# Kernel optimization log

Measured on AMD Instinct MI355X. Metric: run time of the kernel, lower is better.

## Reference

```python
import jax, jax.numpy as jnp
import numpy as np
import math

B, T, C = 2, 2048, 1024
NH = 16
HD = C // NH

def setup_inputs() -> dict:
    key = jax.random.key(0)
    ks = jax.random.split(key, 3)
    scale = 0.02
    return {
        "x": jax.random.normal(ks[0], (B, T, C), dtype=jnp.float32),
        "Wqkv": jax.random.normal(ks[1], (C, 3 * C), dtype=jnp.float32) * scale,
        "bqkv": jnp.zeros((3 * C,), dtype=jnp.float32),
        "Wproj": jax.random.normal(ks[2], (C, C), dtype=jnp.float32) * scale,
        "bproj": jnp.zeros((C,), dtype=jnp.float32),
    }

def reference(x, Wqkv, bqkv, Wproj, bproj):
    b, t, c = x.shape
    qkv = x @ Wqkv + bqkv                      # (B,T,3C)
    qkv = qkv.reshape(b, t, 3, NH, HD)
    q = jnp.transpose(qkv[:, :, 0], (0, 2, 1, 3))  # (B,H,T,D)
    k = jnp.transpose(qkv[:, :, 1], (0, 2, 1, 3))
    v = jnp.transpose(qkv[:, :, 2], (0, 2, 1, 3))
    att = jnp.einsum('bhqd,bhkd->bhqk', q, k) / math.sqrt(HD)
    causal = jnp.tril(jnp.ones((t, t), dtype=bool))
    att = jnp.where(causal[None, None], att, jnp.float32(-jnp.inf))
    att = jax.nn.softmax(att, axis=-1)
    y = jnp.einsum('bhqk,bhkd->bhqd', att, v)  # (B,H,T,D)
    y = jnp.transpose(y, (0, 2, 1, 3)).reshape(b, t, c)
    return y @ Wproj + bproj
```

## Files before the change

kernel.cpp:

```cpp
#include <hip/hip_runtime.h>


typedef __attribute__((ext_vector_type(8))) short short8;
typedef __attribute__((ext_vector_type(4))) float f32x4;
struct ushort4_t { unsigned short x, y, z, w; };

#define MFMA16(a, b, c) __builtin_amdgcn_mfma_f32_16x16x32_bf16((a), (b), (c), 0, 0, 0)

__device__ __forceinline__ unsigned short f2bf(float f) {
  unsigned u = __builtin_bit_cast(unsigned, f);
  u += 0x7fffu + ((u >> 16) & 1u);
  return (unsigned short)(u >> 16);
}

__device__ __forceinline__ unsigned short f2bf_fast(float f) {
  return (unsigned short)((__builtin_bit_cast(unsigned, f) + 0x8000u) >> 16);
}

__device__ __forceinline__ void gl2lds16(const void* g, void* l) {
  __builtin_amdgcn_global_load_lds(
      (__attribute__((address_space(1))) void*)g,
      (__attribute__((address_space(3))) void*)l,
      16, 0, 0);
}

__global__ __launch_bounds__(256) void conv_bf16(const float* __restrict__ src,
                                                 unsigned short* __restrict__ dst,
                                                 int n) {
  int i = (blockIdx.x * 256 + threadIdx.x) * 4;
  if (i >= n) return;
  float4 f = *(const float4*)(src + i);
  unsigned long long r = (unsigned long long)f2bf(f.x)
      | ((unsigned long long)f2bf(f.y) << 16)
      | ((unsigned long long)f2bf(f.z) << 32)
      | ((unsigned long long)f2bf(f.w) << 48);
  *(unsigned long long*)(dst + i) = r;
}

__global__ __launch_bounds__(256) void transpose_conv(const float* __restrict__ W,
                                                      unsigned short* __restrict__ WT,
                                                      int K, int N) {
  __shared__ float tile[64][65];
  const int n0 = blockIdx.x * 64, k0 = blockIdx.y * 64;
  const int tid = threadIdx.x;
  const int c = tid & 63, rbase = tid >> 6;
#pragma unroll
  for (int i = 0; i < 16; ++i) {
    int r = i * 4 + rbase;
    tile[r][c] = W[(size_t)(k0 + r) * N + n0 + c];
  }
  __syncthreads();
#pragma unroll
  for (int i = 0; i < 16; ++i) {
    int r = i * 4 + rbase;
    WT[(size_t)(n0 + r) * K + k0 + c] = f2bf(tile[c][r]);
  }
}

template <int EPI, int MT>
__global__ __launch_bounds__(256)
void gemm_bt(const unsigned short* __restrict__ A,
             const unsigned short* __restrict__ BT,
             const float* __restrict__ bias,
             float* __restrict__ outF,
             unsigned short* __restrict__ q_out,
             unsigned short* __restrict__ k_out,
             unsigned short* __restrict__ vT_out,
             int Ndim, int Kdim) {
  constexpr int IF = MT / 32;
  constexpr int RA = MT / 32;
  __shared__ __align__(16) unsigned short As[MT * 64];
  __shared__ __align__(16) unsigned short Bs[128 * 64];
  const int tid = threadIdx.x;
  const int wave = tid >> 6, lane = tid & 63;
  const int quad = lane >> 4, lr = lane & 15;
  const int wm = wave >> 1, wn = wave & 1;
  const int m0 = blockIdx.y * MT, n0 = blockIdx.x * 128;

  const int r_l = tid >> 3;
  const int cg = (tid & 7) ^ (r_l & 7);
  const unsigned short* gA = A + (size_t)(m0 + r_l) * Kdim + cg * 8;
  const unsigned short* gB = BT + (size_t)(n0 + r_l) * Kdim + cg * 8;
  const size_t rstep = (size_t)32 * Kdim;

  f32x4 acc[IF][4] = {};
  for (int k0 = 0; k0 < Kdim; k0 += 64) {
#pragma unroll
    for (int rd = 0; rd < RA; ++rd)
      gl2lds16(gA + k0 + rd * rstep, As + rd * 2048 + wave * 512);
#pragma unroll
    for (int rd = 0; rd < 4; ++rd)
      gl2lds16(gB + k0 + rd * rstep, Bs + rd * 2048 + wave * 512);
    __syncthreads();
#pragma unroll
    for (int s = 0; s < 2; ++s) {
      const int sw = ((s * 4 + quad) ^ (lr & 7)) * 8;
      short8 a[IF], b[4];
#pragma unroll
      for (int i = 0; i < IF; ++i)
        a[i] = *(const short8*)(As + (wm * (MT / 2) + i * 16 + lr) * 64 + sw);
#pragma unroll
      for (int j = 0; j < 4; ++j)
        b[j] = *(const short8*)(Bs + (wn * 64 + j * 16 + lr) * 64 + sw);
#pragma unroll
      for (int i = 0; i < IF; ++i)
#pragma unroll
        for (int j = 0; j < 4; ++j)
          acc[i][j] = MFMA16(a[i], b[j], acc[i][j]);
    }
    __syncthreads();
  }

  const int row_t = wm * (MT / 2) + quad * 4;
  const int col_t = wn * 64 + lr;
  if (EPI == 0) {
    const int sec = n0 >> 10;
#pragma unroll
    for (int j = 0; j < 4; ++j) {
      const int n = n0 + col_t + j * 16;
      const float bi = bias[n];
      const int nn = n & 1023, h = nn >> 6, d = nn & 63;
#pragma unroll
      for (int i = 0; i < IF; ++i) {
        const int m_base = m0 + row_t + i * 16;
        const int bb = m_base >> 11, t0 = m_base & 2047;
        const int bh = bb * 16 + h;
        if (sec == 2) {
          ushort4_t pk;
          pk.x = f2bf(acc[i][j][0] + bi);
          pk.y = f2bf(acc[i][j][1] + bi);
          pk.z = f2bf(acc[i][j][2] + bi);
          pk.w = f2bf(acc[i][j][3] + bi);
          *(ushort4_t*)(vT_out + ((size_t)bh * 64 + d) * 2048 + t0) = pk;
        } else {
          unsigned short* dst = (sec == 0 ? q_out : k_out) + (size_t)bh * 131072 + t0 * 64 + d;
#pragma unroll
          for (int r = 0; r < 4; ++r)
            dst[r * 64] = f2bf(acc[i][j][r] + bi);
        }
      }
    }
  } else {
#pragma unroll
    for (int i = 0; i < IF; ++i)
#pragma unroll
      for (int r = 0; r < 4; ++r) {
        const int m = m0 + row_t + i * 16 + r;
#pragma unroll
        for (int j = 0; j < 4; ++j) {
          const int n = n0 + col_t + j * 16;
          outF[(size_t)m * Ndim + n] = acc[i][j][r] + bias[n];
        }
      }
  }
}

__global__ __launch_bounds__(256, 4)
void attn(const unsigned short* __restrict__ qbuf,
          const unsigned short* __restrict__ kbuf,
          const unsigned short* __restrict__ vT,
          unsigned short* __restrict__ yb) {
  __shared__ __align__(16) unsigned short Ks[2][4096];
  __shared__ __align__(16) unsigned short Vs[2][4096];
  __shared__ __align__(16) unsigned short Ps[4][1024];
  const int tid = threadIdx.x, wave = tid >> 6, lane = tid & 63;
  const int quad = lane >> 4, lr = lane & 15;
  const int bh = blockIdx.y;
  const int qt = ((int)blockIdx.x + bh) & 31;
  const int qb = qt * 64 + wave * 16;

  const unsigned short* qp0 = qbuf + (size_t)bh * 131072;
  const unsigned short* kp0 = kbuf + (size_t)bh * 131072;
  const unsigned short* vp0 = vT   + (size_t)bh * 131072;

  const unsigned short* qp = qp0 + (size_t)(qb + lr) * 64 + quad * 8;
  const short8 aq0 = *(const short8*)qp;
  const short8 aq1 = *(const short8*)(qp + 32);

  short8 ones;
#pragma unroll
  for (int i = 0; i < 8; ++i) ones[i] = (short)0x3F80;

  const int sr = tid >> 3;
  const int scg = (tid & 7) ^ (sr & 7);
  int kvoff[4][2];
#pragma unroll
  for (int jt = 0; jt < 4; ++jt)
#pragma unroll
    for (int h = 0; h < 2; ++h)
      kvoff[jt][h] = (jt * 16 + lr) * 64 + (((quad + 4 * h) ^ (lr & 7)) << 3);
  int pwoff[4][4];
#pragma unroll
  for (int jt = 0; jt < 4; ++jt)
#pragma unroll
    for (int r = 0; r < 4; ++r) {
      const int row = quad * 4 + r;
      pwoff[jt][r] = row * 64 + (((jt * 2 + (lr >> 3)) ^ (row & 7)) << 3) + (lr & 7);
    }
  const int proff0 = lr * 64 + ((quad ^ (lr & 7)) << 3);
  const int proff1 = lr * 64 + (((quad + 4) ^ (lr & 7)) << 3);

  f32x4 o[4] = {};
  f32x4 lacc = {};
  const float C = 0.18033688f;

  auto stage = [&](int buf, int kt) {
    const unsigned short* kg = kp0 + (size_t)(kt * 64 + sr) * 64 + scg * 8;
    const unsigned short* vg = vp0 + (size_t)sr * 2048 + kt * 64 + scg * 8;
    gl2lds16(kg,             &Ks[buf][wave * 512]);
    gl2lds16(kg + 32 * 64,   &Ks[buf][2048 + wave * 512]);
    gl2lds16(vg,             &Vs[buf][wave * 512]);
    gl2lds16(vg + 32 * 2048, &Vs[buf][2048 + wave * 512]);
  };

  stage(0, 0);
  int buf = 0;
  unsigned short* pw = Ps[wave];
  for (int kt = 0; kt <= qt; ++kt) {
    __syncthreads();
    if (kt < qt) stage(buf ^ 1, kt + 1);
    const unsigned short* Kb = Ks[buf];
    const unsigned short* Vb = Vs[buf];
    short8 bk[4][2];
#pragma unroll
    for (int jt = 0; jt < 4; ++jt) {
      bk[jt][0] = *(const short8*)(Kb + kvoff[jt][0]);
      bk[jt][1] = *(const short8*)(Kb + kvoff[jt][1]);
    }
    f32x4 s[4] = {};
#pragma unroll
    for (int jt = 0; jt < 4; ++jt) {
      s[jt] = MFMA16(aq0, bk[jt][0], s[jt]);
      s[jt] = MFMA16(aq1, bk[jt][1], s[jt]);
    }
    if (kt == qt) {
      const int qr = qb + quad * 4;
#pragma unroll
      for (int jt = 0; jt < 4; ++jt) {
        const int key = kt * 64 + jt * 16 + lr;
#pragma unroll
        for (int r = 0; r < 4; ++r) {
          float p = __builtin_amdgcn_exp2f(s[jt][r] * C);
          if (key > qr + r) p = 0.f;
          pw[pwoff[jt][r]] = f2bf_fast(p);
        }
      }
    } else {
#pragma unroll
      for (int jt = 0; jt < 4; ++jt)
#pragma unroll
        for (int r = 0; r < 4; ++r)
          pw[pwoff[jt][r]] = f2bf_fast(__builtin_amdgcn_exp2f(s[jt][r] * C));
    }
    short8 bv[4][2];
#pragma unroll
    for (int jt = 0; jt < 4; ++jt) {
      bv[jt][0] = *(const short8*)(Vb + kvoff[jt][0]);
      bv[jt][1] = *(const short8*)(Vb + kvoff[jt][1]);
    }
    const short8 ap0 = *(const short8*)(pw + proff0);
    const short8 ap1 = *(const short8*)(pw + proff1);
    lacc = MFMA16(ap0, ones, lacc);
    lacc = MFMA16(ap1, ones, lacc);
#pragma unroll
    for (int jt = 0; jt < 4; ++jt) {
      o[jt] = MFMA16(ap0, bv[jt][0], o[jt]);
      o[jt] = MFMA16(ap1, bv[jt][1], o[jt]);
    }
    buf ^= 1;
  }

  const int b = bh >> 4, h = bh & 15;
  float inv[4];
#pragma unroll
  for (int r = 0; r < 4; ++r) inv[r] = __builtin_amdgcn_rcpf(lacc[r]);
#pragma unroll
  for (int jt = 0; jt < 4; ++jt)
#pragma unroll
    for (int r = 0; r < 4; ++r) {
      const int t = qb + quad * 4 + r;
      yb[((size_t)b * 2048 + t) * 1024 + h * 64 + jt * 16 + lr] =
          f2bf(o[jt][r] * inv[r]);
    }
}

extern "C" void kernel_launch(void* const* d_in, const int* in_sizes, int n_in,
                              void* d_out, int out_size, void* d_ws, size_t ws_size,
                              hipStream_t stream) {
  const float* x     = (const float*)d_in[0];
  const float* Wqkv  = (const float*)d_in[1];
  const float* bqkv  = (const float*)d_in[2];
  const float* Wproj = (const float*)d_in[3];
  const float* bproj = (const float*)d_in[4];
  float* out = (float*)d_out;

  char* ws = (char*)d_ws;
  unsigned short* xb     = (unsigned short*)(ws);
  unsigned short* wqkvT  = (unsigned short*)(ws + 8388608);
  unsigned short* wprojT = (unsigned short*)(ws + 14680064);
  unsigned short* qbuf   = (unsigned short*)(ws + 16777216);
  unsigned short* kbuf   = (unsigned short*)(ws + 25165824);
  unsigned short* vTbuf  = (unsigned short*)(ws + 33554432);
  unsigned short* ybuf   = (unsigned short*)(ws + 41943040);

  conv_bf16<<<4096, 256, 0, stream>>>(x, xb, 4194304);
  transpose_conv<<<dim3(48, 16), 256, 0, stream>>>(Wqkv, wqkvT, 1024, 3072);
  transpose_conv<<<dim3(16, 16), 256, 0, stream>>>(Wproj, wprojT, 1024, 1024);
  gemm_bt<0, 128><<<dim3(24, 32), 256, 0, stream>>>(xb, wqkvT, bqkv, nullptr,
                                                    qbuf, kbuf, vTbuf, 3072, 1024);
  attn<<<dim3(32, 32), 256, 0, stream>>>(qbuf, kbuf, vTbuf, ybuf);
  gemm_bt<1, 64><<<dim3(8, 64), 256, 0, stream>>>(ybuf, wprojT, bproj, out,
                                                  nullptr, nullptr, nullptr, 1024, 1024);
}
```

Measured before the change: 185.6 us.

## Keep attention probabilities in registers via transposed QK^T and K16 MFMA for PV

```diff
diff --git a/kernel.cpp b/kernel.cpp
--- a/kernel.cpp
+++ b/kernel.cpp
@@ -2,10 +2,12 @@
 
 
 typedef __attribute__((ext_vector_type(8))) short short8;
+typedef __attribute__((ext_vector_type(4))) short short4v;
 typedef __attribute__((ext_vector_type(4))) float f32x4;
 struct ushort4_t { unsigned short x, y, z, w; };
 
 #define MFMA16(a, b, c) __builtin_amdgcn_mfma_f32_16x16x32_bf16((a), (b), (c), 0, 0, 0)
+#define MFMA16K16(a, b, c) __builtin_amdgcn_mfma_f32_16x16x16bf16_1k((a), (b), (c), 0, 0, 0)
 
 __device__ __forceinline__ unsigned short f2bf(float f) {
   unsigned u = __builtin_bit_cast(unsigned, f);
@@ -115,6 +117,7 @@
   const int col_t = wn * 64 + lr;
   if (EPI == 0) {
     const int sec = n0 >> 10;
+    const float scl = (sec == 0) ? 0.18033688f : 1.0f;
 #pragma unroll
     for (int j = 0; j < 4; ++j) {
       const int n = n0 + col_t + j * 16;
@@ -136,7 +139,7 @@
           unsigned short* dst = (sec == 0 ? q_out : k_out) + (size_t)bh * 131072 + t0 * 64 + d;
 #pragma unroll
           for (int r = 0; r < 4; ++r)
-            dst[r * 64] = f2bf(acc[i][j][r] + bi);
+            dst[r * 64] = f2bf((acc[i][j][r] + bi) * scl);
         }
       }
     }
@@ -155,14 +158,13 @@
   }
 }
 
-__global__ __launch_bounds__(256, 4)
+__global__ __launch_bounds__(256, 5)
 void attn(const unsigned short* __restrict__ qbuf,
           const unsigned short* __restrict__ kbuf,
           const unsigned short* __restrict__ vT,
           unsigned short* __restrict__ yb) {
   __shared__ __align__(16) unsigned short Ks[2][4096];
   __shared__ __align__(16) unsigned short Vs[2][4096];
-  __shared__ __align__(16) unsigned short Ps[4][1024];
   const int tid = threadIdx.x, wave = tid >> 6, lane = tid & 63;
   const int quad = lane >> 4, lr = lane & 15;
   const int bh = blockIdx.y;
@@ -177,32 +179,19 @@
   const short8 aq0 = *(const short8*)qp;
   const short8 aq1 = *(const short8*)(qp + 32);
 
-  short8 ones;
-#pragma unroll
-  for (int i = 0; i < 8; ++i) ones[i] = (short)0x3F80;
-
   const int sr = tid >> 3;
   const int scg = (tid & 7) ^ (sr & 7);
-  int kvoff[4][2];
-#pragma unroll
-  for (int jt = 0; jt < 4; ++jt)
-#pragma unroll
-    for (int h = 0; h < 2; ++h)
-      kvoff[jt][h] = (jt * 16 + lr) * 64 + (((quad + 4 * h) ^ (lr & 7)) << 3);
-  int pwoff[4][4];
-#pragma unroll
-  for (int jt = 0; jt < 4; ++jt)
-#pragma unroll
-    for (int r = 0; r < 4; ++r) {
-      const int row = quad * 4 + r;
-      pwoff[jt][r] = row * 64 + (((jt * 2 + (lr >> 3)) ^ (row & 7)) << 3) + (lr & 7);
-    }
-  const int proff0 = lr * 64 + ((quad ^ (lr & 7)) << 3);
-  const int proff1 = lr * 64 + (((quad + 4) ^ (lr & 7)) << 3);
+  int kbase[2];
+#pragma unroll
+  for (int h = 0; h < 2; ++h)
+    kbase[h] = lr * 64 + (((quad + 4 * h) ^ (lr & 7)) << 3);
+  int vbase[4];
+#pragma unroll
+  for (int kb = 0; kb < 4; ++kb)
+    vbase[kb] = lr * 64 + (((2 * kb + (quad >> 1)) ^ (lr & 7)) << 3) + (quad & 1) * 4;
 
   f32x4 o[4] = {};
-  f32x4 lacc = {};
-  const float C = 0.18033688f;
+  float lsum = 0.f;
 
   auto stage = [&](int buf, int kt) {
     const unsigned short* kg = kp0 + (size_t)(kt * 64 + sr) * 64 + scg * 8;
@@ -215,7 +204,6 @@
 
   stage(0, 0);
   int buf = 0;
-  unsigned short* pw = Ps[wave];
   for (int kt = 0; kt <= qt; ++kt) {
     __syncthreads();
     if (kt < qt) stage(buf ^ 1, kt + 1);
@@ -224,63 +212,62 @@
     short8 bk[4][2];
 #pragma unroll
     for (int jt = 0; jt < 4; ++jt) {
-      bk[jt][0] = *(const short8*)(Kb + kvoff[jt][0]);
-      bk[jt][1] = *(const short8*)(Kb + kvoff[jt][1]);
+      bk[jt][0] = *(const short8*)(Kb + jt * 1024 + kbase[0]);
+      bk[jt][1] = *(const short8*)(Kb + jt * 1024 + kbase[1]);
     }
     f32x4 s[4] = {};
 #pragma unroll
     for (int jt = 0; jt < 4; ++jt) {
-      s[jt] = MFMA16(aq0, bk[jt][0], s[jt]);
-      s[jt] = MFMA16(aq1, bk[jt][1], s[jt]);
-    }
+      s[jt] = MFMA16(bk[jt][0], aq0, s[jt]);
+      s[jt] = MFMA16(bk[jt][1], aq1, s[jt]);
+    }
+    short4v pa[4];
     if (kt == qt) {
-      const int qr = qb + quad * 4;
-#pragma unroll
-      for (int jt = 0; jt < 4; ++jt) {
-        const int key = kt * 64 + jt * 16 + lr;
+      const int qloc = wave * 16 + lr;
+#pragma unroll
+      for (int jt = 0; jt < 4; ++jt)
 #pragma unroll
         for (int r = 0; r < 4; ++r) {
-          float p = __builtin_amdgcn_exp2f(s[jt][r] * C);
-          if (key > qr + r) p = 0.f;
-          pw[pwoff[jt][r]] = f2bf_fast(p);
+          float p = __builtin_amdgcn_exp2f(s[jt][r]);
+          if (jt * 16 + quad * 4 + r > qloc) p = 0.f;
+          lsum += p;
+          pa[jt][r] = (short)f2bf_fast(p);
         }
+    } else {
+#pragma unroll
+      for (int jt = 0; jt < 4; ++jt)
+#pragma unroll
+        for (int r = 0; r < 4; ++r) {
+          float p = __builtin_amdgcn_exp2f(s[jt][r]);
+          lsum += p;
+          pa[jt][r] = (short)f2bf_fast(p);
+        }
+    }
+#pragma unroll
+    for (int kb = 0; kb < 4; ++kb)
+#pragma unroll
+      for (int jd = 0; jd < 4; ++jd) {
+        const short4v bv = *(const short4v*)(Vb + jd * 1024 + vbase[kb]);
+        o[jd] = MFMA16K16(pa[kb], bv, o[jd]);
       }
-    } else {
-#pragma unroll
-      for (int jt = 0; jt < 4; ++jt)
-#pragma unroll
-        for (int r = 0; r < 4; ++r)
-          pw[pwoff[jt][r]] = f2bf_fast(__builtin_amdgcn_exp2f(s[jt][r] * C));
-    }
-    short8 bv[4][2];
-#pragma unroll
-    for (int jt = 0; jt < 4; ++jt) {
-      bv[jt][0] = *(const short8*)(Vb + kvoff[jt][0]);
-      bv[jt][1] = *(const short8*)(Vb + kvoff[jt][1]);
-    }
-    const short8 ap0 = *(const short8*)(pw + proff0);
-    const short8 ap1 = *(const short8*)(pw + proff1);
-    lacc = MFMA16(ap0, ones, lacc);
-    lacc = MFMA16(ap1, ones, lacc);
-#pragma unroll
-    for (int jt = 0; jt < 4; ++jt) {
-      o[jt] = MFMA16(ap0, bv[jt][0], o[jt]);
-      o[jt] = MFMA16(ap1, bv[jt][1], o[jt]);
-    }
     buf ^= 1;
   }
 
+  lsum += __shfl_xor(lsum, 16);
+  lsum += __shfl_xor(lsum, 32);
+  float inv[4];
+#pragma unroll
+  for (int r = 0; r < 4; ++r)
+    inv[r] = __builtin_amdgcn_rcpf(__shfl(lsum, quad * 4 + r));
+
   const int b = bh >> 4, h = bh & 15;
-  float inv[4];
-#pragma unroll
-  for (int r = 0; r < 4; ++r) inv[r] = __builtin_amdgcn_rcpf(lacc[r]);
-#pragma unroll
-  for (int jt = 0; jt < 4; ++jt)
+#pragma unroll
+  for (int jd = 0; jd < 4; ++jd)
 #pragma unroll
     for (int r = 0; r < 4; ++r) {
       const int t = qb + quad * 4 + r;
-      yb[((size_t)b * 2048 + t) * 1024 + h * 64 + jt * 16 + lr] =
-          f2bf(o[jt][r] * inv[r]);
+      yb[((size_t)b * 2048 + t) * 1024 + h * 64 + jd * 16 + lr] =
+          f2bf(o[jd][r] * inv[r]);
     }
 }
 
```

Measured after the change: 193.0 us. 1.04x slower.
